# Kernel tuning notes

Hardware: AMD Instinct MI355X
Metric: run time of the kernel (lower is better)

Reference implementation:

```python
import jax, jax.numpy as jnp
import numpy as np

B, T, C = 2, 2048, 1024
H, HS = 16, 64
FF = 4 * C
EPS = 1e-5


def _layernorm(x, w):
    mu = jnp.mean(x, axis=-1, keepdims=True)
    var = jnp.var(x, axis=-1, keepdims=True)
    return (x - mu) / jnp.sqrt(var + EPS) * w


def setup_inputs() -> dict:
    key = jax.random.key(0)
    ks = jax.random.split(key, 16)
    s_in = 1.0 / np.sqrt(C)
    s_o = 1.0 / np.sqrt(H * HS)
    s_ff = 1.0 / np.sqrt(FF)
    return {
        "x": jax.random.normal(ks[0], (B, T, C), dtype=jnp.float32),
        "ln1_w": jnp.ones((C,), jnp.float32),
        "Wq": jax.random.uniform(ks[1], (H, C, HS), jnp.float32, -s_in, s_in),
        "bq": jax.random.uniform(ks[2], (H, HS), jnp.float32, -s_in, s_in),
        "Wk": jax.random.uniform(ks[3], (H, C, HS), jnp.float32, -s_in, s_in),
        "bk": jax.random.uniform(ks[4], (H, HS), jnp.float32, -s_in, s_in),
        "Wv": jax.random.uniform(ks[5], (H, C, HS), jnp.float32, -s_in, s_in),
        "bv": jax.random.uniform(ks[6], (H, HS), jnp.float32, -s_in, s_in),
        "Wo": jax.random.uniform(ks[7], (H * HS, C), jnp.float32, -s_o, s_o),
        "bo": jax.random.uniform(ks[8], (C,), jnp.float32, -s_o, s_o),
        "ln2_w": jnp.ones((C,), jnp.float32),
        "W1": jax.random.uniform(ks[9], (C, FF), jnp.float32, -s_in, s_in),
        "b1": jax.random.uniform(ks[10], (FF,), jnp.float32, -s_in, s_in),
        "W2": jax.random.uniform(ks[11], (FF, C), jnp.float32, -s_ff, s_ff),
        "b2": jax.random.uniform(ks[12], (C,), jnp.float32, -s_ff, s_ff),
    }


def reference(x, ln1_w, Wq, bq, Wk, bk, Wv, bv, Wo, bo, ln2_w, W1, b1, W2, b2):
    h = _layernorm(x, ln1_w)                                   # [B,T,C]
    q = jnp.einsum("btc,hcd->bhtd", h, Wq) + bq[:, None, :]    # [B,H,T,HS]
    k = jnp.einsum("btc,hcd->bhtd", h, Wk) + bk[:, None, :]
    v = jnp.einsum("btc,hcd->bhtd", h, Wv) + bv[:, None, :]
    scores = jnp.einsum("bhid,bhjd->bhij", q, k) * (HS ** -0.5)
    causal = jnp.tril(jnp.ones((T, T), bool))                  # tril mask
    scores = jnp.where(causal, scores, -jnp.inf)
    # NOTE: original applies softmax over torch dim=1 of [B,T,T] = query axis i
    w = jax.nn.softmax(scores, axis=2)                         # [B,H,i,j]
    att = jnp.einsum("bhij,bhjd->bhid", w, v)                  # [B,H,T,HS]
    att = att.transpose(0, 2, 1, 3).reshape(B, T, H * HS)      # concat heads
    att = att @ Wo + bo                                        # [B,T,C]
    x1 = x + att
    h2 = _layernorm(x1, ln2_w)
    ff = jax.nn.relu(h2 @ W1 + b1) @ W2 + b2
    return x1 + ff
```

## Files before the change

kernel.cpp:

```cpp
#include <hip/hip_runtime.h>
#include <hip/hip_bf16.h>
#include <stddef.h>
#include <stdint.h>


constexpr int Bn = 2, Tn = 2048, Cn = 1024, Hn = 16, HSn = 64, FFn = 4096;
constexpr int Mn = Bn * Tn;
constexpr float EPSf = 1e-5f;
constexpr float S2 = 0.125f * 1.44269504088896340736f;

using short8 = __attribute__((ext_vector_type(8))) short;
using f32x4  = __attribute__((ext_vector_type(4))) float;
using s16x4  = __attribute__((ext_vector_type(4))) short;

#define DEVINL __device__ __forceinline__

DEVINL unsigned short f2bf(float f) {
  unsigned int u = __float_as_uint(f);
  u += 0x7fffu + ((u >> 16) & 1u);
  return (unsigned short)(u >> 16);
}

#define GLDS16(g, l) __builtin_amdgcn_global_load_lds(                        \
    (const __attribute__((address_space(1))) void*)(g),                       \
    (__attribute__((address_space(3))) void*)(l), 16, 0, 0)

__global__ __launch_bounds__(256)
void transpose_cvt(const float* __restrict__ in, unsigned short* __restrict__ out,
                   int R, int S, long zin, long zout) {
  __shared__ float tile[32][33];
  const int c0 = blockIdx.x * 32;
  const int r0 = blockIdx.y * 32;
  in  += (size_t)blockIdx.z * zin;
  out += (size_t)blockIdx.z * zout;
  const int tid = threadIdx.x;
#pragma unroll
  for (int j = 0; j < 4; ++j) {
    const int f = tid + j * 256;
    tile[f >> 5][f & 31] = in[(size_t)(r0 + (f >> 5)) * S + c0 + (f & 31)];
  }
  __syncthreads();
#pragma unroll
  for (int j = 0; j < 4; ++j) {
    const int f = tid + j * 256;
    const int sr = f >> 5, rc = f & 31;
    out[(size_t)(c0 + sr) * R + r0 + rc] = f2bf(tile[rc][sr]);
  }
}

__global__ __launch_bounds__(256)
void ln_bf16(const float* __restrict__ x, const float* __restrict__ w,
             unsigned short* __restrict__ out) {
  const int row = blockIdx.x, tid = threadIdx.x;
  const float4 v = ((const float4*)(x + (size_t)row * Cn))[tid];
  float s  = v.x + v.y + v.z + v.w;
  float ss = v.x*v.x + v.y*v.y + v.z*v.z + v.w*v.w;
#pragma unroll
  for (int o = 32; o > 0; o >>= 1) { s += __shfl_xor(s, o); ss += __shfl_xor(ss, o); }
  __shared__ float red[8];
  if ((tid & 63) == 0) { red[tid >> 6] = s; red[(tid >> 6) + 4] = ss; }
  __syncthreads();
  s  = red[0] + red[1] + red[2] + red[3];
  ss = red[4] + red[5] + red[6] + red[7];
  const float mu   = s * (1.0f / Cn);
  const float rstd = rsqrtf(ss * (1.0f / Cn) - mu * mu + EPSf);
  const float4 wv = ((const float4*)w)[tid];
  s16x4 o;
  o[0] = (short)f2bf((v.x - mu) * rstd * wv.x);
  o[1] = (short)f2bf((v.y - mu) * rstd * wv.y);
  o[2] = (short)f2bf((v.z - mu) * rstd * wv.z);
  o[3] = (short)f2bf((v.w - mu) * rstd * wv.w);
  ((s16x4*)(out + (size_t)row * Cn))[tid] = o;
}

template <int EPI, int OMODE>
__global__ __launch_bounds__(256)
void gemm_bf16(const unsigned short* __restrict__ A,
               const unsigned short* __restrict__ Bt,
               const float* __restrict__ bias, const float* __restrict__ res,
               void* __restrict__ outp, int M, int N, int K) {
  __shared__ unsigned short As[2][128][64];
  __shared__ unsigned short Bs[2][128][64];
  const int tid = threadIdx.x;
  const int w = tid >> 6, l = tid & 63;
  const int wm = w >> 1, wn = w & 1;
  const int gx = gridDim.x, nwg = gx * gridDim.y;
  int wg = blockIdx.y * gx + blockIdx.x;
  {
    const int q = nwg >> 3, r = nwg & 7;
    const int xcd = wg & 7, off = wg >> 3;
    wg = (xcd < r ? xcd * (q + 1) : r * (q + 1) + (xcd - r) * q) + off;
  }
  const int m0 = (wg / gx) * 128, n0 = (wg % gx) * 128;

  f32x4 acc[4][4];
#pragma unroll
  for (int i = 0; i < 4; ++i)
#pragma unroll
    for (int j = 0; j < 4; ++j) acc[i][j] = (f32x4){0.f, 0.f, 0.f, 0.f};

  const unsigned short* Abase = A + (size_t)m0 * K;
  const unsigned short* Bbase = Bt + (size_t)n0 * K;

  auto STAGE = [&](unsigned short* as, unsigned short* bs, int k0) {
#pragma unroll
    for (int j = 0; j < 4; ++j) {
      const int chunk = (w * 4 + j) * 64 + l;
      const int row = chunk >> 3, slot = chunk & 7;
      const size_t go = (size_t)row * K + k0 + ((slot ^ (row & 7)) << 3);
      GLDS16(Abase + go, as + (size_t)(w * 4 + j) * 512);
      GLDS16(Bbase + go, bs + (size_t)(w * 4 + j) * 512);
    }
  };
  auto COMPUTE = [&](const unsigned short (*as)[64], const unsigned short (*bs)[64]) {
#pragma unroll
    for (int kk = 0; kk < 2; ++kk) {
      short8 a[4], b[4];
#pragma unroll
      for (int i = 0; i < 4; ++i) {
        const int ar = wm * 64 + i * 16 + (l & 15);
        a[i] = *(const short8*)&as[ar][(((l >> 4) + kk * 4) ^ (ar & 7)) << 3];
        const int br = wn * 64 + i * 16 + (l & 15);
        b[i] = *(const short8*)&bs[br][(((l >> 4) + kk * 4) ^ (br & 7)) << 3];
      }
#pragma unroll
      for (int mi = 0; mi < 4; ++mi)
#pragma unroll
        for (int ni = 0; ni < 4; ++ni)
          acc[mi][ni] = __builtin_amdgcn_mfma_f32_16x16x32_bf16(
              a[mi], b[ni], acc[mi][ni], 0, 0, 0);
    }
  };

  const int nt = K >> 6;
  STAGE(&As[0][0][0], &Bs[0][0][0], 0);
  __syncthreads();
  for (int t = 0; t + 2 < nt; t += 2) {
    STAGE(&As[1][0][0], &Bs[1][0][0], (t + 1) << 6);
    COMPUTE(As[0], Bs[0]);
    __syncthreads();
    STAGE(&As[0][0][0], &Bs[0][0][0], (t + 2) << 6);
    COMPUTE(As[1], Bs[1]);
    __syncthreads();
  }
  STAGE(&As[1][0][0], &Bs[1][0][0], (nt - 1) << 6);
  COMPUTE(As[0], Bs[0]);
  __syncthreads();
  COMPUTE(As[1], Bs[1]);

  if (OMODE == 3) {
    if (n0 < 2048) {
      unsigned short* qk = (unsigned short*)outp;
#pragma unroll
      for (int mi = 0; mi < 4; ++mi)
#pragma unroll
        for (int ni = 0; ni < 4; ++ni) {
          const int n = n0 + wn * 64 + ni * 16 + (l & 15);
          const float bv = bias[n];
#pragma unroll
          for (int r = 0; r < 4; ++r) {
            const int m = m0 + wm * 64 + mi * 16 + ((l >> 4) << 2) + r;
            qk[(size_t)m * 2048 + n] = f2bf(acc[mi][ni][r] + bv);
          }
        }
    } else {
      unsigned short* vT = (unsigned short*)outp + (size_t)Mn * 2048;
#pragma unroll
      for (int mi = 0; mi < 4; ++mi)
#pragma unroll
        for (int ni = 0; ni < 4; ++ni) {
          const int n = n0 + wn * 64 + ni * 16 + (l & 15);
          const int nl = n - 2048;
          const int mbase = m0 + wm * 64 + mi * 16 + ((l >> 4) << 2);
          const int bb = mbase >> 11, t = mbase & 2047;
          const float bv = bias[n];
          unsigned short* dst = vT + ((size_t)(bb * 1024 + nl)) * Tn + t;
          unsigned int p0 = (unsigned)f2bf(acc[mi][ni][0] + bv) |
                            ((unsigned)f2bf(acc[mi][ni][1] + bv) << 16);
          unsigned int p1 = (unsigned)f2bf(acc[mi][ni][2] + bv) |
                            ((unsigned)f2bf(acc[mi][ni][3] + bv) << 16);
          *(unsigned int*)dst       = p0;
          *(unsigned int*)(dst + 2) = p1;
        }
    }
  } else {
#pragma unroll
    for (int mi = 0; mi < 4; ++mi)
#pragma unroll
      for (int ni = 0; ni < 4; ++ni) {
        const int n = n0 + wn * 64 + ni * 16 + (l & 15);
        const float bv = bias[n];
#pragma unroll
        for (int r = 0; r < 4; ++r) {
          const int m = m0 + wm * 64 + mi * 16 + ((l >> 4) << 2) + r;
          float v = acc[mi][ni][r] + bv;
          if (EPI == 1) v = fmaxf(v, 0.f);
          if (EPI == 2) v += res[(size_t)m * N + n];
          if (OMODE == 1) ((unsigned short*)outp)[(size_t)m * N + n] = f2bf(v);
          else            ((float*)outp)[(size_t)m * N + n] = v;
        }
      }
  }
}

DEVINL void stage64s(unsigned short* lds, const unsigned short* g, int grs,
                     int w, int l) {
#pragma unroll
  for (int j = 0; j < 2; ++j) {
    const int chunk = (w * 2 + j) * 64 + l;
    const int row = chunk >> 3, slot = chunk & 7;
    GLDS16(g + (size_t)row * grs + ((slot ^ (row & 7)) << 3),
           lds + (size_t)(w * 2 + j) * 512);
  }
}

__global__ __launch_bounds__(256)
void colstats_mfma(const unsigned short* __restrict__ qk,
                   float* __restrict__ m2buf, float* __restrict__ rlbuf) {
  __shared__ unsigned short Ks[64][64];
  __shared__ unsigned short Qs[64][64];
  __shared__ float redm[4][4][16], redl[4][4][16];
  const int j0 = blockIdx.x * 64;
  const int bh = blockIdx.y, b = bh >> 4, h = bh & 15;
  const int tid = threadIdx.x, w = tid >> 6, l = tid & 63;
  const unsigned short* kbase = qk + ((size_t)(b * Tn + j0)) * 2048 + 1024 + h * 64;
  const unsigned short* qbase = qk + ((size_t)(b * Tn)) * 2048 + h * 64;
  stage64s(&Ks[0][0], kbase, 2048, w, l);
  float m2[4], ls[4];
#pragma unroll
  for (int ni = 0; ni < 4; ++ni) { m2[ni] = -1e30f; ls[ni] = 0.f; }

  for (int i0 = j0; i0 < Tn; i0 += 64) {
    __syncthreads();
    stage64s(&Qs[0][0], qbase + (size_t)i0 * 2048, 2048, w, l);
    __syncthreads();
    f32x4 s[4];
#pragma unroll
    for (int ni = 0; ni < 4; ++ni) s[ni] = (f32x4){0.f, 0.f, 0.f, 0.f};
#pragma unroll
    for (int kk = 0; kk < 2; ++kk) {
      const int ar = w * 16 + (l & 15);
      const short8 af = *(const short8*)&Qs[ar][(((l >> 4) + kk * 4) ^ (ar & 7)) << 3];
#pragma unroll
      for (int ni = 0; ni < 4; ++ni) {
        const int br = ni * 16 + (l & 15);
        const short8 bfr = *(const short8*)&Ks[br][(((l >> 4) + kk * 4) ^ (br & 7)) << 3];
        s[ni] = __builtin_amdgcn_mfma_f32_16x16x32_bf16(af, bfr, s[ni], 0, 0, 0);
      }
    }
    const bool diag = (i0 == j0);
    const int ib = w * 16 + ((l >> 4) << 2);
#pragma unroll
    for (int ni = 0; ni < 4; ++ni) {
      const int jl = ni * 16 + (l & 15);
      float v0 = s[ni][0] * S2, v1 = s[ni][1] * S2, v2 = s[ni][2] * S2, v3 = s[ni][3] * S2;
      if (!diag) {
        const float tmax = fmaxf(fmaxf(v0, v1), fmaxf(v2, v3));
        const float mn = fmaxf(m2[ni], tmax);
        ls[ni] = ls[ni] * exp2f(m2[ni] - mn) +
                 exp2f(v0 - mn) + exp2f(v1 - mn) + exp2f(v2 - mn) + exp2f(v3 - mn);
        m2[ni] = mn;
      } else {
        const bool g0 = (ib + 0 >= jl), g1 = (ib + 1 >= jl), g2 = (ib + 2 >= jl), g3 = (ib + 3 >= jl);
        const float t0 = g0 ? v0 : -1e30f, t1 = g1 ? v1 : -1e30f;
        const float t2 = g2 ? v2 : -1e30f, t3 = g3 ? v3 : -1e30f;
        const float tmax = fmaxf(fmaxf(t0, t1), fmaxf(t2, t3));
        const float mn = fmaxf(m2[ni], tmax);
        const float e0 = g0 ? exp2f(v0 - mn) : 0.f;
        const float e1 = g1 ? exp2f(v1 - mn) : 0.f;
        const float e2 = g2 ? exp2f(v2 - mn) : 0.f;
        const float e3 = g3 ? exp2f(v3 - mn) : 0.f;
        ls[ni] = ls[ni] * exp2f(m2[ni] - mn) + e0 + e1 + e2 + e3;
        m2[ni] = mn;
      }
    }
  }
#pragma unroll
  for (int ni = 0; ni < 4; ++ni) {
#pragma unroll
    for (int off = 16; off < 64; off <<= 1) {
      const float mo = __shfl_xor(m2[ni], off);
      const float lo = __shfl_xor(ls[ni], off);
      const float mn = fmaxf(m2[ni], mo);
      ls[ni] = ls[ni] * exp2f(m2[ni] - mn) + lo * exp2f(mo - mn);
      m2[ni] = mn;
    }
  }
  if (l < 16) {
#pragma unroll
    for (int ni = 0; ni < 4; ++ni) { redm[w][ni][l] = m2[ni]; redl[w][ni][l] = ls[ni]; }
  }
  __syncthreads();
  if (tid < 64) {
    const int ni = tid >> 4, jl = tid & 15;
    float m = redm[0][ni][jl], sl = redl[0][ni][jl];
#pragma unroll
    for (int wv = 1; wv < 4; ++wv) {
      const float mo = redm[wv][ni][jl], lo = redl[wv][ni][jl];
      const float mn = fmaxf(m, mo);
      sl = sl * exp2f(m - mn) + lo * exp2f(mo - mn);
      m = mn;
    }
    m2buf[(size_t)bh * Tn + j0 + ni * 16 + jl] = m;
    rlbuf[(size_t)bh * Tn + j0 + ni * 16 + jl] = 1.0f / sl;
  }
}

__global__ __launch_bounds__(256)
void pv_mfma(const unsigned short* __restrict__ qk,
             const unsigned short* __restrict__ vT,
             const float* __restrict__ m2buf, const float* __restrict__ rlbuf,
             unsigned short* __restrict__ att) {
  __shared__ unsigned short Qs[64][64];
  __shared__ unsigned short Ks[64][64];
  __shared__ unsigned short Vs[64][64];
  __shared__ unsigned short Ps[64][64];
  __shared__ float m2s[64], rls[64];
  const int i0 = blockIdx.x * 64;
  const int bh = blockIdx.y, b = bh >> 4, h = bh & 15;
  const int tid = threadIdx.x, w = tid >> 6, l = tid & 63;
  const unsigned short* qbase = qk + ((size_t)(b * Tn + i0)) * 2048 + h * 64;
  const unsigned short* kbase = qk + ((size_t)(b * Tn)) * 2048 + 1024 + h * 64;
  const unsigned short* vbase = vT + ((size_t)(b * 1024 + h * 64)) * Tn;
  stage64s(&Qs[0][0], qbase, 2048, w, l);
  f32x4 oacc[4];
#pragma unroll
  for (int ni = 0; ni < 4; ++ni) oacc[ni] = (f32x4){0.f, 0.f, 0.f, 0.f};

  for (int j0 = 0; j0 <= i0; j0 += 64) {
    __syncthreads();
    stage64s(&Ks[0][0], kbase + (size_t)j0 * 2048, 2048, w, l);
#pragma unroll
    for (int j = 0; j < 2; ++j) {
      const int chunk = (w * 2 + j) * 64 + l;
      const int row = chunk >> 3, slot = chunk & 7;
      GLDS16(vbase + (size_t)row * Tn + j0 + ((slot ^ (row & 7)) << 3),
             &Vs[0][0] + (size_t)(w * 2 + j) * 512);
    }
    if (tid < 64) {
      m2s[tid] = m2buf[(size_t)bh * Tn + j0 + tid];
      rls[tid] = rlbuf[(size_t)bh * Tn + j0 + tid];
    }
    __syncthreads();
    f32x4 s[4];
#pragma unroll
    for (int ni = 0; ni < 4; ++ni) s[ni] = (f32x4){0.f, 0.f, 0.f, 0.f};
#pragma unroll
    for (int kk = 0; kk < 2; ++kk) {
      const int ar = w * 16 + (l & 15);
      const short8 af = *(const short8*)&Qs[ar][(((l >> 4) + kk * 4) ^ (ar & 7)) << 3];
#pragma unroll
      for (int ni = 0; ni < 4; ++ni) {
        const int br = ni * 16 + (l & 15);
        const short8 bfr = *(const short8*)&Ks[br][(((l >> 4) + kk * 4) ^ (br & 7)) << 3];
        s[ni] = __builtin_amdgcn_mfma_f32_16x16x32_bf16(af, bfr, s[ni], 0, 0, 0);
      }
    }
    const bool diag = (j0 == i0);
    const int ib = w * 16 + ((l >> 4) << 2);
    unsigned short* Pf = &Ps[0][0];
#pragma unroll
    for (int ni = 0; ni < 4; ++ni) {
      const int jl = ni * 16 + (l & 15);
      const float mj = m2s[jl], rj = rls[jl];
#pragma unroll
      for (int r = 0; r < 4; ++r) {
        float p = exp2f(s[ni][r] * S2 - mj) * rj;
        if (diag && (ib + r < jl)) p = 0.f;
        const int il = ib + r;
        Pf[il * 64 + (((jl >> 3) ^ (il & 7)) << 3) + (jl & 7)] = f2bf(p);
      }
    }
#pragma unroll
    for (int kk = 0; kk < 2; ++kk) {
      const int ar = w * 16 + (l & 15);
      const short8 pf = *(const short8*)&Ps[ar][(((l >> 4) + kk * 4) ^ (ar & 7)) << 3];
#pragma unroll
      for (int ni = 0; ni < 4; ++ni) {
        const int br = ni * 16 + (l & 15);
        const short8 vf = *(const short8*)&Vs[br][(((l >> 4) + kk * 4) ^ (br & 7)) << 3];
        oacc[ni] = __builtin_amdgcn_mfma_f32_16x16x32_bf16(pf, vf, oacc[ni], 0, 0, 0);
      }
    }
  }
#pragma unroll
  for (int ni = 0; ni < 4; ++ni) {
    const int col = h * 64 + ni * 16 + (l & 15);
#pragma unroll
    for (int r = 0; r < 4; ++r) {
      const int m = b * Tn + i0 + w * 16 + ((l >> 4) << 2) + r;
      att[(size_t)m * 1024 + col] = f2bf(oacc[ni][r]);
    }
  }
}

extern "C" void kernel_launch(void* const* d_in, const int* in_sizes, int n_in,
                              void* d_out, int out_size, void* d_ws, size_t ws_size,
                              hipStream_t stream) {
  const float* x    = (const float*)d_in[0];
  const float* ln1w = (const float*)d_in[1];
  const float* Wq   = (const float*)d_in[2];
  const float* bq   = (const float*)d_in[3];
  const float* Wk   = (const float*)d_in[4];
  const float* bk   = (const float*)d_in[5];
  const float* Wv   = (const float*)d_in[6];
  const float* bv   = (const float*)d_in[7];
  const float* Wo   = (const float*)d_in[8];
  const float* bo   = (const float*)d_in[9];
  const float* ln2w = (const float*)d_in[10];
  const float* W1   = (const float*)d_in[11];
  const float* b1   = (const float*)d_in[12];
  const float* W2   = (const float*)d_in[13];
  const float* b2   = (const float*)d_in[14];

  uint8_t* wsb = (uint8_t*)d_ws;
  unsigned short* h     = (unsigned short*)(wsb);
  unsigned short* qkb   = (unsigned short*)(wsb + (8ull  << 20));
  unsigned short* vT    = (unsigned short*)(wsb + (24ull << 20));
  unsigned short* attb  = (unsigned short*)(wsb + (32ull << 20));
  float*          x1    = (float*)         (wsb + (40ull << 20));
  unsigned short* ffmid = qkb;
  unsigned short* Wqkvt = (unsigned short*)(wsb + (56ull << 20));
  unsigned short* Wot   = (unsigned short*)(wsb + (62ull << 20));
  unsigned short* W1t   = (unsigned short*)(wsb + (64ull << 20));
  unsigned short* W2t   = (unsigned short*)(wsb + (72ull << 20));
  float*          biasqkv=(float*)         (wsb + (80ull << 20));
  float*          m2buf = (float*)         (wsb + (81ull << 20));
  float*          rlbuf = (float*)         (wsb + (81ull << 20) + (256ull << 10));

  transpose_cvt<<<dim3(2, 32, 16), 256, 0, stream>>>(Wq, Wqkvt,                  1024, 64, 65536, 65536);
  transpose_cvt<<<dim3(2, 32, 16), 256, 0, stream>>>(Wk, Wqkvt + 1024 * 1024,    1024, 64, 65536, 65536);
  transpose_cvt<<<dim3(2, 32, 16), 256, 0, stream>>>(Wv, Wqkvt + 2 * 1024 * 1024, 1024, 64, 65536, 65536);
  transpose_cvt<<<dim3(32, 32, 1), 256, 0, stream>>>(Wo, Wot,  1024, 1024, 0, 0);
  transpose_cvt<<<dim3(128, 32, 1), 256, 0, stream>>>(W1, W1t, 1024, 4096, 0, 0);
  transpose_cvt<<<dim3(32, 128, 1), 256, 0, stream>>>(W2, W2t, 4096, 1024, 0, 0);
  hipMemcpyAsync(biasqkv,        bq, 1024 * sizeof(float), hipMemcpyDeviceToDevice, stream);
  hipMemcpyAsync(biasqkv + 1024, bk, 1024 * sizeof(float), hipMemcpyDeviceToDevice, stream);
  hipMemcpyAsync(biasqkv + 2048, bv, 1024 * sizeof(float), hipMemcpyDeviceToDevice, stream);

  ln_bf16<<<Mn, 256, 0, stream>>>(x, ln1w, h);
  gemm_bf16<0, 3><<<dim3(24, 32), 256, 0, stream>>>(h, Wqkvt, biasqkv, nullptr, qkb, Mn, 3072, Cn);
  colstats_mfma<<<dim3(Tn / 64, Bn * Hn), 256, 0, stream>>>(qkb, m2buf, rlbuf);
  pv_mfma<<<dim3(Tn / 64, Bn * Hn), 256, 0, stream>>>(qkb, vT, m2buf, rlbuf, attb);
  gemm_bf16<2, 0><<<dim3(8, 32), 256, 0, stream>>>(attb, Wot, bo, x, x1, Mn, 1024, Cn);
  ln_bf16<<<Mn, 256, 0, stream>>>(x1, ln2w, h);
  gemm_bf16<1, 1><<<dim3(32, 32), 256, 0, stream>>>(h, W1t, b1, nullptr, ffmid, Mn, FFn, Cn);
  gemm_bf16<2, 0><<<dim3(8, 32), 256, 0, stream>>>(ffmid, W2t, b2, x1, (float*)d_out, Mn, Cn, FFn);
}
```

Measured before the change: 482.7 us.

## Balance causal attention blocks, split-K the FFN down GEMM, single-buffer wide GEMMs

The column-stats and PV attention kernels now pair tile bx with tile 31-bx in each block. This halves the grid and evens out the triangular causal work across blocks. The W2 GEMM is split along K into two slices that atomically add into an output pre-filled with residual plus bias by a new init kernel, which doubles its block count from 256. The QKV and W1 GEMMs switch to a single LDS buffer with a synchronous load/compute loop, cutting shared memory in the hope of higher occupancy but losing load/compute overlap. Atomic float adds make the summation order nondeterministic.

```diff
diff --git a/kernel.cpp b/kernel.cpp
--- a/kernel.cpp
+++ b/kernel.cpp
@@ -73,14 +73,25 @@
   ((s16x4*)(out + (size_t)row * Cn))[tid] = o;
 }
 
-template <int EPI, int OMODE>
+__global__ __launch_bounds__(256)
+void init_out(const float* __restrict__ b2, const float* __restrict__ x1,
+              float* __restrict__ out) {
+  const int idx = blockIdx.x * 256 + threadIdx.x;
+  const float4 xv = ((const float4*)x1)[idx];
+  const float4 bb = ((const float4*)b2)[idx & 255];
+  float4 o;
+  o.x = xv.x + bb.x; o.y = xv.y + bb.y; o.z = xv.z + bb.z; o.w = xv.w + bb.w;
+  ((float4*)out)[idx] = o;
+}
+
+template <int EPI, int OMODE, int PIPE>
 __global__ __launch_bounds__(256)
 void gemm_bf16(const unsigned short* __restrict__ A,
                const unsigned short* __restrict__ Bt,
                const float* __restrict__ bias, const float* __restrict__ res,
                void* __restrict__ outp, int M, int N, int K) {
-  __shared__ unsigned short As[2][128][64];
-  __shared__ unsigned short Bs[2][128][64];
+  __shared__ unsigned short As[PIPE + 1][128][64];
+  __shared__ unsigned short Bs[PIPE + 1][128][64];
   const int tid = threadIdx.x;
   const int w = tid >> 6, l = tid & 63;
   const int wm = w >> 1, wn = w & 1;
@@ -92,6 +103,8 @@
     wg = (xcd < r ? xcd * (q + 1) : r * (q + 1) + (xcd - r) * q) + off;
   }
   const int m0 = (wg / gx) * 128, n0 = (wg % gx) * 128;
+  const int kpb = K / gridDim.z;
+  const int kbase = blockIdx.z * kpb;
 
   f32x4 acc[4][4];
 #pragma unroll
@@ -99,8 +112,8 @@
 #pragma unroll
     for (int j = 0; j < 4; ++j) acc[i][j] = (f32x4){0.f, 0.f, 0.f, 0.f};
 
-  const unsigned short* Abase = A + (size_t)m0 * K;
-  const unsigned short* Bbase = Bt + (size_t)n0 * K;
+  const unsigned short* Abase = A + (size_t)m0 * K + kbase;
+  const unsigned short* Bbase = Bt + (size_t)n0 * K + kbase;
 
   auto STAGE = [&](unsigned short* as, unsigned short* bs, int k0) {
 #pragma unroll
@@ -132,21 +145,30 @@
     }
   };
 
-  const int nt = K >> 6;
-  STAGE(&As[0][0][0], &Bs[0][0][0], 0);
-  __syncthreads();
-  for (int t = 0; t + 2 < nt; t += 2) {
-    STAGE(&As[1][0][0], &Bs[1][0][0], (t + 1) << 6);
+  const int nt = kpb >> 6;
+  if (PIPE == 1) {
+    STAGE(&As[0][0][0], &Bs[0][0][0], 0);
+    __syncthreads();
+    for (int t = 0; t + 2 < nt; t += 2) {
+      STAGE(&As[1][0][0], &Bs[1][0][0], (t + 1) << 6);
+      COMPUTE(As[0], Bs[0]);
+      __syncthreads();
+      STAGE(&As[0][0][0], &Bs[0][0][0], (t + 2) << 6);
+      COMPUTE(As[1], Bs[1]);
+      __syncthreads();
+    }
+    STAGE(&As[1][0][0], &Bs[1][0][0], (nt - 1) << 6);
     COMPUTE(As[0], Bs[0]);
     __syncthreads();
-    STAGE(&As[0][0][0], &Bs[0][0][0], (t + 2) << 6);
     COMPUTE(As[1], Bs[1]);
-    __syncthreads();
-  }
-  STAGE(&As[1][0][0], &Bs[1][0][0], (nt - 1) << 6);
-  COMPUTE(As[0], Bs[0]);
-  __syncthreads();
-  COMPUTE(As[1], Bs[1]);
+  } else {
+    for (int t = 0; t < nt; ++t) {
+      if (t) __syncthreads();
+      STAGE(&As[0][0][0], &Bs[0][0][0], t << 6);
+      __syncthreads();
+      COMPUTE(As[0], Bs[0]);
+    }
+  }
 
   if (OMODE == 3) {
     if (n0 < 2048) {
@@ -189,15 +211,19 @@
 #pragma unroll
       for (int ni = 0; ni < 4; ++ni) {
         const int n = n0 + wn * 64 + ni * 16 + (l & 15);
-        const float bv = bias[n];
+        const float bv = (EPI == 3) ? 0.f : bias[n];
 #pragma unroll
         for (int r = 0; r < 4; ++r) {
           const int m = m0 + wm * 64 + mi * 16 + ((l >> 4) << 2) + r;
-          float v = acc[mi][ni][r] + bv;
-          if (EPI == 1) v = fmaxf(v, 0.f);
-          if (EPI == 2) v += res[(size_t)m * N + n];
-          if (OMODE == 1) ((unsigned short*)outp)[(size_t)m * N + n] = f2bf(v);
-          else            ((float*)outp)[(size_t)m * N + n] = v;
+          if (EPI == 3) {
+            unsafeAtomicAdd(&((float*)outp)[(size_t)m * N + n], acc[mi][ni][r]);
+          } else {
+            float v = acc[mi][ni][r] + bv;
+            if (EPI == 1) v = fmaxf(v, 0.f);
+            if (EPI == 2) v += res[(size_t)m * N + n];
+            if (OMODE == 1) ((unsigned short*)outp)[(size_t)m * N + n] = f2bf(v);
+            else            ((float*)outp)[(size_t)m * N + n] = v;
+          }
         }
       }
   }
@@ -220,89 +246,95 @@
   __shared__ unsigned short Ks[64][64];
   __shared__ unsigned short Qs[64][64];
   __shared__ float redm[4][4][16], redl[4][4][16];
-  const int j0 = blockIdx.x * 64;
+  const int bx = blockIdx.x;
   const int bh = blockIdx.y, b = bh >> 4, h = bh & 15;
   const int tid = threadIdx.x, w = tid >> 6, l = tid & 63;
-  const unsigned short* kbase = qk + ((size_t)(b * Tn + j0)) * 2048 + 1024 + h * 64;
   const unsigned short* qbase = qk + ((size_t)(b * Tn)) * 2048 + h * 64;
-  stage64s(&Ks[0][0], kbase, 2048, w, l);
-  float m2[4], ls[4];
-#pragma unroll
-  for (int ni = 0; ni < 4; ++ni) { m2[ni] = -1e30f; ls[ni] = 0.f; }
-
-  for (int i0 = j0; i0 < Tn; i0 += 64) {
+
+  for (int half = 0; half < 2; ++half) {
+    const int jt = half ? (31 - bx) : bx;
+    const int j0 = jt * 64;
+    const unsigned short* kbase = qk + ((size_t)(b * Tn + j0)) * 2048 + 1024 + h * 64;
+    stage64s(&Ks[0][0], kbase, 2048, w, l);
+    float m2[4], ls[4];
+#pragma unroll
+    for (int ni = 0; ni < 4; ++ni) { m2[ni] = -1e30f; ls[ni] = 0.f; }
+
+    for (int i0 = j0; i0 < Tn; i0 += 64) {
+      __syncthreads();
+      stage64s(&Qs[0][0], qbase + (size_t)i0 * 2048, 2048, w, l);
+      __syncthreads();
+      f32x4 s[4];
+#pragma unroll
+      for (int ni = 0; ni < 4; ++ni) s[ni] = (f32x4){0.f, 0.f, 0.f, 0.f};
+#pragma unroll
+      for (int kk = 0; kk < 2; ++kk) {
+        const int ar = w * 16 + (l & 15);
+        const short8 af = *(const short8*)&Qs[ar][(((l >> 4) + kk * 4) ^ (ar & 7)) << 3];
+#pragma unroll
+        for (int ni = 0; ni < 4; ++ni) {
+          const int br = ni * 16 + (l & 15);
+          const short8 bfr = *(const short8*)&Ks[br][(((l >> 4) + kk * 4) ^ (br & 7)) << 3];
+          s[ni] = __builtin_amdgcn_mfma_f32_16x16x32_bf16(af, bfr, s[ni], 0, 0, 0);
+        }
+      }
+      const bool diag = (i0 == j0);
+      const int ib = w * 16 + ((l >> 4) << 2);
+#pragma unroll
+      for (int ni = 0; ni < 4; ++ni) {
+        const int jl = ni * 16 + (l & 15);
+        float v0 = s[ni][0] * S2, v1 = s[ni][1] * S2, v2 = s[ni][2] * S2, v3 = s[ni][3] * S2;
+        if (!diag) {
+          const float tmax = fmaxf(fmaxf(v0, v1), fmaxf(v2, v3));
+          const float mn = fmaxf(m2[ni], tmax);
+          ls[ni] = ls[ni] * exp2f(m2[ni] - mn) +
+                   exp2f(v0 - mn) + exp2f(v1 - mn) + exp2f(v2 - mn) + exp2f(v3 - mn);
+          m2[ni] = mn;
+        } else {
+          const bool g0 = (ib + 0 >= jl), g1 = (ib + 1 >= jl), g2 = (ib + 2 >= jl), g3 = (ib + 3 >= jl);
+          const float t0 = g0 ? v0 : -1e30f, t1 = g1 ? v1 : -1e30f;
+          const float t2 = g2 ? v2 : -1e30f, t3 = g3 ? v3 : -1e30f;
+          const float tmax = fmaxf(fmaxf(t0, t1), fmaxf(t2, t3));
+          const float mn = fmaxf(m2[ni], tmax);
+          const float e0 = g0 ? exp2f(v0 - mn) : 0.f;
+          const float e1 = g1 ? exp2f(v1 - mn) : 0.f;
+          const float e2 = g2 ? exp2f(v2 - mn) : 0.f;
+          const float e3 = g3 ? exp2f(v3 - mn) : 0.f;
+          ls[ni] = ls[ni] * exp2f(m2[ni] - mn) + e0 + e1 + e2 + e3;
+          m2[ni] = mn;
+        }
+      }
+    }
+#pragma unroll
+    for (int ni = 0; ni < 4; ++ni) {
+#pragma unroll
+      for (int off = 16; off < 64; off <<= 1) {
+        const float mo = __shfl_xor(m2[ni], off);
+        const float lo = __shfl_xor(ls[ni], off);
+        const float mn = fmaxf(m2[ni], mo);
+        ls[ni] = ls[ni] * exp2f(m2[ni] - mn) + lo * exp2f(mo - mn);
+        m2[ni] = mn;
+      }
+    }
+    if (l < 16) {
+#pragma unroll
+      for (int ni = 0; ni < 4; ++ni) { redm[w][ni][l] = m2[ni]; redl[w][ni][l] = ls[ni]; }
+    }
     __syncthreads();
-    stage64s(&Qs[0][0], qbase + (size_t)i0 * 2048, 2048, w, l);
+    if (tid < 64) {
+      const int ni = tid >> 4, jl = tid & 15;
+      float m = redm[0][ni][jl], sl = redl[0][ni][jl];
+#pragma unroll
+      for (int wv = 1; wv < 4; ++wv) {
+        const float mo = redm[wv][ni][jl], lo = redl[wv][ni][jl];
+        const float mn = fmaxf(m, mo);
+        sl = sl * exp2f(m - mn) + lo * exp2f(mo - mn);
+        m = mn;
+      }
+      m2buf[(size_t)bh * Tn + j0 + ni * 16 + jl] = m;
+      rlbuf[(size_t)bh * Tn + j0 + ni * 16 + jl] = 1.0f / sl;
+    }
     __syncthreads();
-    f32x4 s[4];
-#pragma unroll
-    for (int ni = 0; ni < 4; ++ni) s[ni] = (f32x4){0.f, 0.f, 0.f, 0.f};
-#pragma unroll
-    for (int kk = 0; kk < 2; ++kk) {
-      const int ar = w * 16 + (l & 15);
-      const short8 af = *(const short8*)&Qs[ar][(((l >> 4) + kk * 4) ^ (ar & 7)) << 3];
-#pragma unroll
-      for (int ni = 0; ni < 4; ++ni) {
-        const int br = ni * 16 + (l & 15);
-        const short8 bfr = *(const short8*)&Ks[br][(((l >> 4) + kk * 4) ^ (br & 7)) << 3];
-        s[ni] = __builtin_amdgcn_mfma_f32_16x16x32_bf16(af, bfr, s[ni], 0, 0, 0);
-      }
-    }
-    const bool diag = (i0 == j0);
-    const int ib = w * 16 + ((l >> 4) << 2);
-#pragma unroll
-    for (int ni = 0; ni < 4; ++ni) {
-      const int jl = ni * 16 + (l & 15);
-      float v0 = s[ni][0] * S2, v1 = s[ni][1] * S2, v2 = s[ni][2] * S2, v3 = s[ni][3] * S2;
-      if (!diag) {
-        const float tmax = fmaxf(fmaxf(v0, v1), fmaxf(v2, v3));
-        const float mn = fmaxf(m2[ni], tmax);
-        ls[ni] = ls[ni] * exp2f(m2[ni] - mn) +
-                 exp2f(v0 - mn) + exp2f(v1 - mn) + exp2f(v2 - mn) + exp2f(v3 - mn);
-        m2[ni] = mn;
-      } else {
-        const bool g0 = (ib + 0 >= jl), g1 = (ib + 1 >= jl), g2 = (ib + 2 >= jl), g3 = (ib + 3 >= jl);
-        const float t0 = g0 ? v0 : -1e30f, t1 = g1 ? v1 : -1e30f;
-        const float t2 = g2 ? v2 : -1e30f, t3 = g3 ? v3 : -1e30f;
-        const float tmax = fmaxf(fmaxf(t0, t1), fmaxf(t2, t3));
-        const float mn = fmaxf(m2[ni], tmax);
-        const float e0 = g0 ? exp2f(v0 - mn) : 0.f;
-        const float e1 = g1 ? exp2f(v1 - mn) : 0.f;
-        const float e2 = g2 ? exp2f(v2 - mn) : 0.f;
-        const float e3 = g3 ? exp2f(v3 - mn) : 0.f;
-        ls[ni] = ls[ni] * exp2f(m2[ni] - mn) + e0 + e1 + e2 + e3;
-        m2[ni] = mn;
-      }
-    }
-  }
-#pragma unroll
-  for (int ni = 0; ni < 4; ++ni) {
-#pragma unroll
-    for (int off = 16; off < 64; off <<= 1) {
-      const float mo = __shfl_xor(m2[ni], off);
-      const float lo = __shfl_xor(ls[ni], off);
-      const float mn = fmaxf(m2[ni], mo);
-      ls[ni] = ls[ni] * exp2f(m2[ni] - mn) + lo * exp2f(mo - mn);
-      m2[ni] = mn;
-    }
-  }
-  if (l < 16) {
-#pragma unroll
-    for (int ni = 0; ni < 4; ++ni) { redm[w][ni][l] = m2[ni]; redl[w][ni][l] = ls[ni]; }
-  }
-  __syncthreads();
-  if (tid < 64) {
-    const int ni = tid >> 4, jl = tid & 15;
-    float m = redm[0][ni][jl], sl = redl[0][ni][jl];
-#pragma unroll
-    for (int wv = 1; wv < 4; ++wv) {
-      const float mo = redm[wv][ni][jl], lo = redl[wv][ni][jl];
-      const float mn = fmaxf(m, mo);
-      sl = sl * exp2f(m - mn) + lo * exp2f(mo - mn);
-      m = mn;
-    }
-    m2buf[(size_t)bh * Tn + j0 + ni * 16 + jl] = m;
-    rlbuf[(size_t)bh * Tn + j0 + ni * 16 + jl] = 1.0f / sl;
   }
 }
 
@@ -316,80 +348,86 @@
   __shared__ unsigned short Vs[64][64];
   __shared__ unsigned short Ps[64][64];
   __shared__ float m2s[64], rls[64];
-  const int i0 = blockIdx.x * 64;
+  const int bx = blockIdx.x;
   const int bh = blockIdx.y, b = bh >> 4, h = bh & 15;
   const int tid = threadIdx.x, w = tid >> 6, l = tid & 63;
-  const unsigned short* qbase = qk + ((size_t)(b * Tn + i0)) * 2048 + h * 64;
   const unsigned short* kbase = qk + ((size_t)(b * Tn)) * 2048 + 1024 + h * 64;
   const unsigned short* vbase = vT + ((size_t)(b * 1024 + h * 64)) * Tn;
-  stage64s(&Qs[0][0], qbase, 2048, w, l);
-  f32x4 oacc[4];
-#pragma unroll
-  for (int ni = 0; ni < 4; ++ni) oacc[ni] = (f32x4){0.f, 0.f, 0.f, 0.f};
-
-  for (int j0 = 0; j0 <= i0; j0 += 64) {
+
+  for (int half = 0; half < 2; ++half) {
+    const int it = half ? (31 - bx) : bx;
+    const int i0 = it * 64;
+    const unsigned short* qbase = qk + ((size_t)(b * Tn + i0)) * 2048 + h * 64;
     __syncthreads();
-    stage64s(&Ks[0][0], kbase + (size_t)j0 * 2048, 2048, w, l);
-#pragma unroll
-    for (int j = 0; j < 2; ++j) {
-      const int chunk = (w * 2 + j) * 64 + l;
-      const int row = chunk >> 3, slot = chunk & 7;
-      GLDS16(vbase + (size_t)row * Tn + j0 + ((slot ^ (row & 7)) << 3),
-             &Vs[0][0] + (size_t)(w * 2 + j) * 512);
-    }
-    if (tid < 64) {
-      m2s[tid] = m2buf[(size_t)bh * Tn + j0 + tid];
-      rls[tid] = rlbuf[(size_t)bh * Tn + j0 + tid];
-    }
-    __syncthreads();
-    f32x4 s[4];
-#pragma unroll
-    for (int ni = 0; ni < 4; ++ni) s[ni] = (f32x4){0.f, 0.f, 0.f, 0.f};
-#pragma unroll
-    for (int kk = 0; kk < 2; ++kk) {
-      const int ar = w * 16 + (l & 15);
-      const short8 af = *(const short8*)&Qs[ar][(((l >> 4) + kk * 4) ^ (ar & 7)) << 3];
+    stage64s(&Qs[0][0], qbase, 2048, w, l);
+    f32x4 oacc[4];
+#pragma unroll
+    for (int ni = 0; ni < 4; ++ni) oacc[ni] = (f32x4){0.f, 0.f, 0.f, 0.f};
+
+    for (int j0 = 0; j0 <= i0; j0 += 64) {
+      __syncthreads();
+      stage64s(&Ks[0][0], kbase + (size_t)j0 * 2048, 2048, w, l);
+#pragma unroll
+      for (int j = 0; j < 2; ++j) {
+        const int chunk = (w * 2 + j) * 64 + l;
+        const int row = chunk >> 3, slot = chunk & 7;
+        GLDS16(vbase + (size_t)row * Tn + j0 + ((slot ^ (row & 7)) << 3),
+               &Vs[0][0] + (size_t)(w * 2 + j) * 512);
+      }
+      if (tid < 64) {
+        m2s[tid] = m2buf[(size_t)bh * Tn + j0 + tid];
+        rls[tid] = rlbuf[(size_t)bh * Tn + j0 + tid];
+      }
+      __syncthreads();
+      f32x4 s[4];
+#pragma unroll
+      for (int ni = 0; ni < 4; ++ni) s[ni] = (f32x4){0.f, 0.f, 0.f, 0.f};
+#pragma unroll
+      for (int kk = 0; kk < 2; ++kk) {
+        const int ar = w * 16 + (l & 15);
+        const short8 af = *(const short8*)&Qs[ar][(((l >> 4) + kk * 4) ^ (ar & 7)) << 3];
+#pragma unroll
+        for (int ni = 0; ni < 4; ++ni) {
+          const int br = ni * 16 + (l & 15);
+          const short8 bfr = *(const short8*)&Ks[br][(((l >> 4) + kk * 4) ^ (br & 7)) << 3];
+          s[ni] = __builtin_amdgcn_mfma_f32_16x16x32_bf16(af, bfr, s[ni], 0, 0, 0);
+        }
+      }
+      const bool diag = (j0 == i0);
+      const int ib = w * 16 + ((l >> 4) << 2);
+      unsigned short* Pf = &Ps[0][0];
 #pragma unroll
       for (int ni = 0; ni < 4; ++ni) {
-        const int br = ni * 16 + (l & 15);
-        const short8 bfr = *(const short8*)&Ks[br][(((l >> 4) + kk * 4) ^ (br & 7)) << 3];
-        s[ni] = __builtin_amdgcn_mfma_f32_16x16x32_bf16(af, bfr, s[ni], 0, 0, 0);
-      }
-    }
-    const bool diag = (j0 == i0);
-    const int ib = w * 16 + ((l >> 4) << 2);
-    unsigned short* Pf = &Ps[0][0];
+        const int jl = ni * 16 + (l & 15);
+        const float mj = m2s[jl], rj = rls[jl];
+#pragma unroll
+        for (int r = 0; r < 4; ++r) {
+          float p = exp2f(s[ni][r] * S2 - mj) * rj;
+          if (diag && (ib + r < jl)) p = 0.f;
+          const int il = ib + r;
+          Pf[il * 64 + (((jl >> 3) ^ (il & 7)) << 3) + (jl & 7)] = f2bf(p);
+        }
+      }
+#pragma unroll
+      for (int kk = 0; kk < 2; ++kk) {
+        const int ar = w * 16 + (l & 15);
+        const short8 pf = *(const short8*)&Ps[ar][(((l >> 4) + kk * 4) ^ (ar & 7)) << 3];
+#pragma unroll
+        for (int ni = 0; ni < 4; ++ni) {
+          const int br = ni * 16 + (l & 15);
+          const short8 vf = *(const short8*)&Vs[br][(((l >> 4) + kk * 4) ^ (br & 7)) << 3];
+          oacc[ni] = __builtin_amdgcn_mfma_f32_16x16x32_bf16(pf, vf, oacc[ni], 0, 0, 0);
+        }
+      }
+    }
 #pragma unroll
     for (int ni = 0; ni < 4; ++ni) {
-      const int jl = ni * 16 + (l & 15);
-      const float mj = m2s[jl], rj = rls[jl];
+      const int col = h * 64 + ni * 16 + (l & 15);
 #pragma unroll
       for (int r = 0; r < 4; ++r) {
-        float p = exp2f(s[ni][r] * S2 - mj) * rj;
-        if (diag && (ib + r < jl)) p = 0.f;
-        const int il = ib + r;
-        Pf[il * 64 + (((jl >> 3) ^ (il & 7)) << 3) + (jl & 7)] = f2bf(p);
-      }
-    }
-#pragma unroll
-    for (int kk = 0; kk < 2; ++kk) {
-      const int ar = w * 16 + (l & 15);
-      const short8 pf = *(const short8*)&Ps[ar][(((l >> 4) + kk * 4) ^ (ar & 7)) << 3];
-#pragma unroll
-      for (int ni = 0; ni < 4; ++ni) {
-        const int br = ni * 16 + (l & 15);
-        const short8 vf = *(const short8*)&Vs[br][(((l >> 4) + kk * 4) ^ (br & 7)) << 3];
-        oacc[ni] = __builtin_amdgcn_mfma_f32_16x16x32_bf16(pf, vf, oacc[ni], 0, 0, 0);
-      }
-    }
-  }
-#pragma unroll
-  for (int ni = 0; ni < 4; ++ni) {
-    const int col = h * 64 + ni * 16 + (l & 15);
-#pragma unroll
-    for (int r = 0; r < 4; ++r) {
-      const int m = b * Tn + i0 + w * 16 + ((l >> 4) << 2) + r;
-      att[(size_t)m * 1024 + col] = f2bf(oacc[ni][r]);
+        const int m = b * Tn + i0 + w * 16 + ((l >> 4) << 2) + r;
+        att[(size_t)m * 1024 + col] = f2bf(oacc[ni][r]);
+      }
     }
   }
 }
@@ -439,11 +477,12 @@
   hipMemcpyAsync(biasqkv + 2048, bv, 1024 * sizeof(float), hipMemcpyDeviceToDevice, stream);
 
   ln_bf16<<<Mn, 256, 0, stream>>>(x, ln1w, h);
-  gemm_bf16<0, 3><<<dim3(24, 32), 256, 0, stream>>>(h, Wqkvt, biasqkv, nullptr, qkb, Mn, 3072, Cn);
-  colstats_mfma<<<dim3(Tn / 64, Bn * Hn), 256, 0, stream>>>(qkb, m2buf, rlbuf);
-  pv_mfma<<<dim3(Tn / 64, Bn * Hn), 256, 0, stream>>>(qkb, vT, m2buf, rlbuf, attb);
-  gemm_bf16<2, 0><<<dim3(8, 32), 256, 0, stream>>>(attb, Wot, bo, x, x1, Mn, 1024, Cn);
+  gemm_bf16<0, 3, 0><<<dim3(24, 32), 256, 0, stream>>>(h, Wqkvt, biasqkv, nullptr, qkb, Mn, 3072, Cn);
+  colstats_mfma<<<dim3(16, Bn * Hn), 256, 0, stream>>>(qkb, m2buf, rlbuf);
+  pv_mfma<<<dim3(16, Bn * Hn), 256, 0, stream>>>(qkb, vT, m2buf, rlbuf, attb);
+  gemm_bf16<2, 0, 1><<<dim3(8, 32), 256, 0, stream>>>(attb, Wot, bo, x, x1, Mn, 1024, Cn);
   ln_bf16<<<Mn, 256, 0, stream>>>(x1, ln2w, h);
-  gemm_bf16<1, 1><<<dim3(32, 32), 256, 0, stream>>>(h, W1t, b1, nullptr, ffmid, Mn, FFn, Cn);
-  gemm_bf16<2, 0><<<dim3(8, 32), 256, 0, stream>>>(ffmid, W2t, b2, x1, (float*)d_out, Mn, Cn, FFn);
-}
+  gemm_bf16<1, 1, 0><<<dim3(32, 32), 256, 0, stream>>>(h, W1t, b1, nullptr, ffmid, Mn, FFn, Cn);
+  init_out<<<Mn * Cn / 1024, 256, 0, stream>>>(b2, x1, (float*)d_out);
+  gemm_bf16<3, 0, 1><<<dim3(8, 32, 2), 256, 0, stream>>>(ffmid, W2t, nullptr, nullptr, (float*)d_out, Mn, Cn, FFn);
+}
```

Result: faster. 423.0 us (-12.4%).
